# Optimization experiments

Measured on AMD Instinct MI355X. Metric: run time of the kernel, lower is better.

Reference implementation:

```python
import jax, jax.numpy as jnp
import numpy as np

K_TOP = 16
SPLITS = 16


def setup_inputs() -> dict:
    key = jax.random.key(0)
    kq, kt = jax.random.split(key)
    queries = jax.random.normal(kq, (4096, 128), dtype=jnp.float32)
    table = jax.random.normal(kt, (4096, 128, 128), dtype=jnp.float32)
    return {"queries": queries, "table": table}


def reference(queries, table):
    n_queries, vector_dim = queries.shape
    rows, scores_per_row, _ = table.shape
    table_size = rows * scores_per_row
    queries_per_split = n_queries // SPLITS
    q_split = queries.reshape(SPLITS, queries_per_split, vector_dim)
    row_offsets = jnp.arange(0, table_size, scores_per_row)  # [rows]

    def split_top_k(split_queries):
        # scores: [q, rows, values_per_row]
        split_scores = jnp.einsum('qd,rvd->qrv', split_queries, table)
        top_id_by_row = jnp.argmax(split_scores, axis=-1)        # [q, rows]
        top_score_by_row = jnp.max(split_scores, axis=-1)        # [q, rows]
        # top-k rows by per-row max score (descending)
        top_row_idx = jnp.argsort(top_score_by_row, axis=-1)[:, :-K_TOP - 1:-1]  # [q, k]
        # matmul_slice == gather along axis -1 (one-hot matmul trick on TPU)
        ids_by_topk_row = jnp.take_along_axis(top_id_by_row, top_row_idx, axis=-1)  # [q, k]
        split_topk_values = table[top_row_idx, ids_by_topk_row]  # [q, k, d]
        top_table_id_by_row = top_id_by_row + row_offsets        # [q, rows]
        split_topk_ids = jnp.take_along_axis(top_table_id_by_row, top_row_idx, axis=-1)
        split_topk_scores = jnp.take_along_axis(top_score_by_row, top_row_idx, axis=-1)
        return split_topk_values, split_topk_scores, split_topk_ids

    topk_values, topk_scores, topk_ids = jax.lax.map(split_top_k, q_split)
    topk_values = topk_values.reshape(n_queries, K_TOP, -1)
    topk_scores = topk_scores.reshape(n_queries, K_TOP)
    topk_ids = topk_ids.reshape(n_queries, K_TOP)
    return topk_values, topk_scores, topk_ids
```

## Files before the change

### kernel.cpp

```cpp
#include <hip/hip_runtime.h>
#include <stdint.h>


typedef __attribute__((ext_vector_type(8))) short short8;
typedef __attribute__((ext_vector_type(4))) float floatx4;
typedef __attribute__((ext_vector_type(16))) float floatx16;
typedef unsigned long long u64;
typedef unsigned int u32;

#define NQ 4096
#define NR 4096
#define NV 128
#define ND 128
#define KTOP 16
#define RC 16
#define NCHUNK (NR / RC)
#define CPC 8
#define CSEL 24
#define BCAP 1024

__device__ __forceinline__ unsigned short f2bf(float f) {
  u32 u = __float_as_uint(f);
  u32 r = u + 0x7FFFu + ((u >> 16) & 1u);
  return (unsigned short)(r >> 16);
}
__device__ __forceinline__ u32 key_of(float s) {
  u32 b = __float_as_uint(s);
  return (b & 0x80000000u) ? ~b : (b | 0x80000000u);
}
__device__ __forceinline__ float unkey(u32 k) {
  u32 b = (k & 0x80000000u) ? (k & 0x7FFFFFFFu) : ~k;
  return __uint_as_float(b);
}
__device__ __forceinline__ void glds16(const void* g, void* l) {
  __builtin_amdgcn_global_load_lds(
      (const __attribute__((address_space(1))) unsigned int*)g,
      (__attribute__((address_space(3))) unsigned int*)l, 16, 0, 0);
}
__device__ __forceinline__ float max16(floatx16 a) {
  float m0 = fmaxf(fmaxf(a[0], a[1]), fmaxf(a[2], a[3]));
  float m1 = fmaxf(fmaxf(a[4], a[5]), fmaxf(a[6], a[7]));
  float m2 = fmaxf(fmaxf(a[8], a[9]), fmaxf(a[10], a[11]));
  float m3 = fmaxf(fmaxf(a[12], a[13]), fmaxf(a[14], a[15]));
  return fmaxf(fmaxf(m0, m1), fmaxf(m2, m3));
}
__device__ __forceinline__ void insert8(u64* a, u64 x) {
  if (x > a[CPC - 1]) {
#pragma unroll
    for (int p = 0; p < CPC; p++) {
      u64 mx = a[p] > x ? a[p] : x;
      u64 mn = a[p] > x ? x : a[p];
      a[p] = mx; x = mn;
    }
  }
}

__global__ void k0_convert(const float* __restrict__ t, unsigned short* __restrict__ o) {
  size_t i = ((size_t)blockIdx.x * 256 + threadIdx.x) * 4;
  float4 v = *reinterpret_cast<const float4*>(t + i);
  ushort4 r;
  r.x = f2bf(v.x); r.y = f2bf(v.y); r.z = f2bf(v.z); r.w = f2bf(v.w);
  *reinterpret_cast<ushort4*>(o + i) = r;
}

__launch_bounds__(256, 2)
__global__ void k1_coarse(const float* __restrict__ Q, const unsigned short* __restrict__ T16,
                          u64* __restrict__ cand) {
  __shared__ short Blds[2][128 * 128];

  const int tid = threadIdx.x;
  const int wave = tid >> 6;
  const int lane = tid & 63;
  const int l31 = lane & 31;
  const int l15 = lane & 15;
  const int half = lane >> 5;
  const int qblock = blockIdx.x;
  const int chunk = blockIdx.y;

  short8 bf0[8], bf1[8];
  {
    const float* qp0 = Q + (size_t)(qblock * 256 + wave * 64 + l31) * 128;
    const float* qp1 = qp0 + 32 * 128;
#pragma unroll
    for (int kb = 0; kb < 8; kb++) {
      float4 x = *reinterpret_cast<const float4*>(qp0 + kb * 16 + half * 8);
      float4 y = *reinterpret_cast<const float4*>(qp0 + kb * 16 + half * 8 + 4);
      short8 b;
      b[0] = (short)f2bf(x.x); b[1] = (short)f2bf(x.y);
      b[2] = (short)f2bf(x.z); b[3] = (short)f2bf(x.w);
      b[4] = (short)f2bf(y.x); b[5] = (short)f2bf(y.y);
      b[6] = (short)f2bf(y.z); b[7] = (short)f2bf(y.w);
      bf0[kb] = b;
      x = *reinterpret_cast<const float4*>(qp1 + kb * 16 + half * 8);
      y = *reinterpret_cast<const float4*>(qp1 + kb * 16 + half * 8 + 4);
      b[0] = (short)f2bf(x.x); b[1] = (short)f2bf(x.y);
      b[2] = (short)f2bf(x.z); b[3] = (short)f2bf(x.w);
      b[4] = (short)f2bf(y.x); b[5] = (short)f2bf(y.y);
      b[6] = (short)f2bf(y.z); b[7] = (short)f2bf(y.w);
      bf1[kb] = b;
    }
  }

  int goff[8];
#pragma unroll
  for (int i = 0; i < 8; i++) {
    int v = wave * 32 + i * 4 + (lane >> 4);
    int kb = l15 ^ (v & 15);
    goff[i] = v * 256 + kb * 16;
  }
  const char* chunkbase = (const char*)(T16 + (size_t)(chunk * RC) * (NV * ND));

#pragma unroll
  for (int i = 0; i < 8; i++)
    glds16(chunkbase + goff[i], &Blds[0][(wave * 8 + i) * 512 + lane * 8]);
  __syncthreads();

  u64 a0[CPC], a1[CPC];
#pragma unroll
  for (int i = 0; i < CPC; i++) { a0[i] = 0; a1[i] = 0; }

  const short* abase = &Blds[0][l31 * 128];
  for (int rl = 0; rl < RC; rl++) {
    const int cur = rl & 1;
    if (rl < RC - 1) {
      const char* rs = chunkbase + (size_t)(rl + 1) * 32768;
#pragma unroll
      for (int i = 0; i < 8; i++)
        glds16(rs + goff[i], &Blds[1 - cur][(wave * 8 + i) * 512 + lane * 8]);
    }

    float run0 = -3.402823466e+38f, run1 = -3.402823466e+38f;
#pragma unroll
    for (int t = 0; t < 4; t++) {
      floatx16 acc0 = 0, acc1 = 0;
#pragma unroll
      for (int kb = 0; kb < 8; kb++) {
        const short* ap = abase + cur * 16384 + t * 4096 +
                          8 * ((kb * 2 + half) ^ (l31 & 15));
        short8 af = *reinterpret_cast<const short8*>(ap);
        acc0 = __builtin_amdgcn_mfma_f32_32x32x16_bf16(af, bf0[kb], acc0, 0, 0, 0);
        acc1 = __builtin_amdgcn_mfma_f32_32x32x16_bf16(af, bf1[kb], acc1, 0, 0, 0);
      }
      run0 = fmaxf(run0, max16(acc0));
      run1 = fmaxf(run1, max16(acc1));
    }
    run0 = fmaxf(run0, __shfl_xor(run0, 32, 64));
    run1 = fmaxf(run1, __shfl_xor(run1, 32, 64));

    u32 rid = (u32)(chunk * RC + rl);
    insert8(a0, ((u64)key_of(run0) << 32) | rid);
    insert8(a1, ((u64)key_of(run1) << 32) | rid);
    __syncthreads();
  }

  if (lane < 32) {
    const int q0 = qblock * 256 + wave * 64 + l31;
    u64* dst0 = cand + (size_t)q0 * (NCHUNK * CPC) + chunk * CPC;
    u64* dst1 = dst0 + (size_t)32 * (NCHUNK * CPC);
#pragma unroll
    for (int i = 0; i < CPC; i++) { dst0[i] = a0[i]; dst1[i] = a1[i]; }
  }
}

__global__ void k2_select(const u64* __restrict__ cand, u64* __restrict__ refined,
                          u32* __restrict__ cnt, u32* __restrict__ bucket) {
  const int q = blockIdx.x;
  const int lane = threadIdx.x;
  const u64* base = cand + (size_t)q * (NCHUNK * CPC);
  u64 a[12];
#pragma unroll
  for (int i = 0; i < 12; i++) a[i] = 0;
  for (int i = 0; i < 32; i++) {
    u64 x = base[i * 64 + lane];
    if (x > a[11]) {
#pragma unroll
      for (int p = 0; p < 12; p++) {
        u64 mx = a[p] > x ? a[p] : x;
        u64 mn = a[p] > x ? x : a[p];
        a[p] = mx; x = mn;
      }
    }
  }
  if (lane < CSEL) refined[(size_t)q * CSEL + lane] = 0;

  for (int j = 0; j < CSEL; j++) {
    u64 head = a[0];
    u64 W = head;
#pragma unroll
    for (int off = 1; off < 64; off <<= 1) {
      u64 o = __shfl_xor(W, off, 64);
      if (o > W) W = o;
    }
    if (head == W) {
#pragma unroll
      for (int p = 0; p < 11; p++) a[p] = a[p + 1];
      a[11] = 0;
      u32 row = (u32)W & 4095u;
      u32 slot = atomicAdd(cnt + row, 1u);
      if (slot < BCAP) bucket[(size_t)row * BCAP + slot] = ((u32)q << 5) | (u32)j;
    }
  }
}

__device__ __forceinline__ void k3_emit(float acc, u32 ent, int row, int v, int lane,
                                        u64* __restrict__ refined) {
  u64 p = ((u64)key_of(acc) << 32) | (u32)(127 - v);
#pragma unroll
  for (int off = 1; off < 64; off <<= 1) {
    u64 o = __shfl_xor(p, off, 64);
    if (o > p) p = o;
  }
  if (lane == 0) {
    u32 q = ent >> 5, j = ent & 31u;
    u32 vbest = 127u - (u32)(p & 0xFFFFFFFFu);
    u64 packed = ((p >> 32) << 32) | (u32)(row * 128 + vbest);
    atomicMax(reinterpret_cast<unsigned long long*>(&refined[(size_t)q * CSEL + j]), packed);
  }
}

__global__ void k3_refine(const float* __restrict__ Q, const float* __restrict__ table,
                          const u32* __restrict__ cnt, const u32* __restrict__ bucket,
                          u64* __restrict__ refined) {
  __shared__ float rowv[128 * 128];
  const int row = blockIdx.x;
  const int tid = threadIdx.x;
  u32 n = cnt[row];
  if (n > BCAP) n = BCAP;
  if (n == 0) return;
  const float* src = table + (size_t)row * (NV * ND);
#pragma unroll
  for (int i = 0; i < 16; i++) {
    int idx = i * 1024 + tid * 4;
    int v = idx >> 7;
    int d4 = tid & 31;
    *reinterpret_cast<float4*>(&rowv[v * 128 + ((d4 ^ (v & 31)) << 2)]) =
        *reinterpret_cast<const float4*>(src + idx);
  }
  __syncthreads();
  const int g = tid >> 7;
  const int v = tid & 127;
  const int lane = tid & 63;
  const int sw = v & 31;
  const u32* bk = bucket + (size_t)row * BCAP;
  for (u32 e0 = (u32)(g * 4); e0 < n; e0 += 8) {
    u32 ent0 = __builtin_amdgcn_readfirstlane(bk[e0]);
    u32 ent1 = __builtin_amdgcn_readfirstlane(bk[e0 + 1 < n ? e0 + 1 : e0]);
    u32 ent2 = __builtin_amdgcn_readfirstlane(bk[e0 + 2 < n ? e0 + 2 : e0]);
    u32 ent3 = __builtin_amdgcn_readfirstlane(bk[e0 + 3 < n ? e0 + 3 : e0]);
    const float* qp0 = Q + (size_t)(ent0 >> 5) * 128;
    const float* qp1 = Q + (size_t)(ent1 >> 5) * 128;
    const float* qp2 = Q + (size_t)(ent2 >> 5) * 128;
    const float* qp3 = Q + (size_t)(ent3 >> 5) * 128;
    float c0 = 0.f, c1 = 0.f, c2 = 0.f, c3 = 0.f;
#pragma unroll
    for (int d4 = 0; d4 < 32; d4++) {
      float4 rv = *reinterpret_cast<const float4*>(&rowv[v * 128 + ((d4 ^ sw) << 2)]);
      c0 = fmaf(rv.x, qp0[d4 * 4 + 0], c0);
      c0 = fmaf(rv.y, qp0[d4 * 4 + 1], c0);
      c0 = fmaf(rv.z, qp0[d4 * 4 + 2], c0);
      c0 = fmaf(rv.w, qp0[d4 * 4 + 3], c0);
      c1 = fmaf(rv.x, qp1[d4 * 4 + 0], c1);
      c1 = fmaf(rv.y, qp1[d4 * 4 + 1], c1);
      c1 = fmaf(rv.z, qp1[d4 * 4 + 2], c1);
      c1 = fmaf(rv.w, qp1[d4 * 4 + 3], c1);
      c2 = fmaf(rv.x, qp2[d4 * 4 + 0], c2);
      c2 = fmaf(rv.y, qp2[d4 * 4 + 1], c2);
      c2 = fmaf(rv.z, qp2[d4 * 4 + 2], c2);
      c2 = fmaf(rv.w, qp2[d4 * 4 + 3], c2);
      c3 = fmaf(rv.x, qp3[d4 * 4 + 0], c3);
      c3 = fmaf(rv.y, qp3[d4 * 4 + 1], c3);
      c3 = fmaf(rv.z, qp3[d4 * 4 + 2], c3);
      c3 = fmaf(rv.w, qp3[d4 * 4 + 3], c3);
    }
    k3_emit(c0, ent0, row, v, lane, refined);
    if (e0 + 1 < n) k3_emit(c1, ent1, row, v, lane, refined);
    if (e0 + 2 < n) k3_emit(c2, ent2, row, v, lane, refined);
    if (e0 + 3 < n) k3_emit(c3, ent3, row, v, lane, refined);
  }
}

__global__ void k4_finalize(const float* __restrict__ table, const u64* __restrict__ refined,
                            float* __restrict__ out) {
  __shared__ u64 arr[CSEL];
  __shared__ u32 fids[KTOP];
  __shared__ float scs[KTOP];
  const int q = blockIdx.x;
  const int tid = threadIdx.x;
  if (tid < CSEL) arr[tid] = refined[(size_t)q * CSEL + tid];
  __syncthreads();
  if (tid == 0) {
    for (int i = 1; i < CSEL; i++) {
      u64 x = arr[i]; int p = i;
      while (p > 0 && arr[p - 1] < x) { arr[p] = arr[p - 1]; p--; }
      arr[p] = x;
    }
    for (int i = 0; i < KTOP; i++) {
      fids[i] = (u32)arr[i];
      scs[i] = unkey((u32)(arr[i] >> 32));
    }
  }
  __syncthreads();
  const int i = tid >> 4, sub = tid & 15;
  const float* src = table + (size_t)fids[i] * 128 + sub * 8;
  float* dst = out + ((size_t)q * KTOP + i) * 128 + sub * 8;
  *reinterpret_cast<float4*>(dst) = *reinterpret_cast<const float4*>(src);
  *reinterpret_cast<float4*>(dst + 4) = *reinterpret_cast<const float4*>(src + 4);
  if (tid < KTOP) {
    out[8388608 + (size_t)q * KTOP + tid] = scs[tid];
    out[8388608 + 65536 + (size_t)q * KTOP + tid] = (float)fids[tid];
  }
}

extern "C" void kernel_launch(void* const* d_in, const int* in_sizes, int n_in,
                              void* d_out, int out_size, void* d_ws, size_t ws_size,
                              hipStream_t stream) {
  (void)in_sizes; (void)n_in; (void)out_size; (void)ws_size;
  const float* Q = (const float*)d_in[0];
  const float* T = (const float*)d_in[1];
  float* out = (float*)d_out;
  char* ws = (char*)d_ws;
  unsigned short* T16 = (unsigned short*)ws;
  u64* cand    = (u64*)(ws + 134217728);
  u32* cnt     = (u32*)(ws + 134217728 + 67108864);
  u32* bucket  = (u32*)(ws + 134217728 + 67108864 + 16384);
  u64* refined = (u64*)(ws + 134217728 + 67108864 + 16384 + 16777216);

  hipMemsetAsync(cnt, 0, NR * sizeof(u32), stream);
  k0_convert<<<65536, 256, 0, stream>>>(T, T16);
  k1_coarse<<<dim3(16, 256), 256, 0, stream>>>(Q, T16, cand);
  k2_select<<<NQ, 64, 0, stream>>>(cand, refined, cnt, bucket);
  k3_refine<<<NR, 256, 0, stream>>>(Q, T, cnt, bucket, refined);
  k4_finalize<<<NQ, 256, 0, stream>>>(T, refined, out);
}
```

Baseline: 1.316 ms.

## Raise MFMA wave priority in coarse kernel; refine one entry per wave-group with 512 threads

The coarse-scoring kernel now raises wave priority around its MFMA inner loop so that matrix issue is favoured over the other waves. The refine kernel moves from 256 threads, where each 128-thread group handled four bucket entries at once, to 512 threads where each group handles a single entry per iteration. This gives more concurrent waves and less register pressure, but each shared-memory row read is reused across fewer queries. The tile load loop is adjusted to match the larger block.

Result: faster. 1.184 ms (-10.1%).

```diff
diff --git a/kernel.cpp b/kernel.cpp
--- a/kernel.cpp
+++ b/kernel.cpp
@@ -133,6 +133,7 @@
 #pragma unroll
     for (int t = 0; t < 4; t++) {
       floatx16 acc0 = 0, acc1 = 0;
+      __builtin_amdgcn_s_setprio(1);
 #pragma unroll
       for (int kb = 0; kb < 8; kb++) {
         const short* ap = abase + cur * 16384 + t * 4096 +
@@ -141,6 +142,7 @@
         acc0 = __builtin_amdgcn_mfma_f32_32x32x16_bf16(af, bf0[kb], acc0, 0, 0, 0);
         acc1 = __builtin_amdgcn_mfma_f32_32x32x16_bf16(af, bf1[kb], acc1, 0, 0, 0);
       }
+      __builtin_amdgcn_s_setprio(0);
       run0 = fmaxf(run0, max16(acc0));
       run1 = fmaxf(run1, max16(acc1));
     }
@@ -199,22 +201,6 @@
       u32 slot = atomicAdd(cnt + row, 1u);
       if (slot < BCAP) bucket[(size_t)row * BCAP + slot] = ((u32)q << 5) | (u32)j;
     }
-  }
-}
-
-__device__ __forceinline__ void k3_emit(float acc, u32 ent, int row, int v, int lane,
-                                        u64* __restrict__ refined) {
-  u64 p = ((u64)key_of(acc) << 32) | (u32)(127 - v);
-#pragma unroll
-  for (int off = 1; off < 64; off <<= 1) {
-    u64 o = __shfl_xor(p, off, 64);
-    if (o > p) p = o;
-  }
-  if (lane == 0) {
-    u32 q = ent >> 5, j = ent & 31u;
-    u32 vbest = 127u - (u32)(p & 0xFFFFFFFFu);
-    u64 packed = ((p >> 32) << 32) | (u32)(row * 128 + vbest);
-    atomicMax(reinterpret_cast<unsigned long long*>(&refined[(size_t)q * CSEL + j]), packed);
   }
 }
 
@@ -229,53 +215,41 @@
   if (n == 0) return;
   const float* src = table + (size_t)row * (NV * ND);
 #pragma unroll
-  for (int i = 0; i < 16; i++) {
-    int idx = i * 1024 + tid * 4;
+  for (int i = 0; i < 8; i++) {
+    int idx = i * 2048 + tid * 4;
     int v = idx >> 7;
     int d4 = tid & 31;
     *reinterpret_cast<float4*>(&rowv[v * 128 + ((d4 ^ (v & 31)) << 2)]) =
         *reinterpret_cast<const float4*>(src + idx);
   }
   __syncthreads();
-  const int g = tid >> 7;
   const int v = tid & 127;
   const int lane = tid & 63;
   const int sw = v & 31;
-  const u32* bk = bucket + (size_t)row * BCAP;
-  for (u32 e0 = (u32)(g * 4); e0 < n; e0 += 8) {
-    u32 ent0 = __builtin_amdgcn_readfirstlane(bk[e0]);
-    u32 ent1 = __builtin_amdgcn_readfirstlane(bk[e0 + 1 < n ? e0 + 1 : e0]);
-    u32 ent2 = __builtin_amdgcn_readfirstlane(bk[e0 + 2 < n ? e0 + 2 : e0]);
-    u32 ent3 = __builtin_amdgcn_readfirstlane(bk[e0 + 3 < n ? e0 + 3 : e0]);
-    const float* qp0 = Q + (size_t)(ent0 >> 5) * 128;
-    const float* qp1 = Q + (size_t)(ent1 >> 5) * 128;
-    const float* qp2 = Q + (size_t)(ent2 >> 5) * 128;
-    const float* qp3 = Q + (size_t)(ent3 >> 5) * 128;
-    float c0 = 0.f, c1 = 0.f, c2 = 0.f, c3 = 0.f;
+  for (u32 ei = (u32)(tid >> 7); ei < n; ei += 4) {
+    u32 ent = __builtin_amdgcn_readfirstlane(bucket[(size_t)row * BCAP + ei]);
+    u32 q = ent >> 5, j = ent & 31u;
+    const float* qp = Q + (size_t)q * 128;
+    float acc = 0.f;
 #pragma unroll
     for (int d4 = 0; d4 < 32; d4++) {
       float4 rv = *reinterpret_cast<const float4*>(&rowv[v * 128 + ((d4 ^ sw) << 2)]);
-      c0 = fmaf(rv.x, qp0[d4 * 4 + 0], c0);
-      c0 = fmaf(rv.y, qp0[d4 * 4 + 1], c0);
-      c0 = fmaf(rv.z, qp0[d4 * 4 + 2], c0);
-      c0 = fmaf(rv.w, qp0[d4 * 4 + 3], c0);
-      c1 = fmaf(rv.x, qp1[d4 * 4 + 0], c1);
-      c1 = fmaf(rv.y, qp1[d4 * 4 + 1], c1);
-      c1 = fmaf(rv.z, qp1[d4 * 4 + 2], c1);
-      c1 = fmaf(rv.w, qp1[d4 * 4 + 3], c1);
-      c2 = fmaf(rv.x, qp2[d4 * 4 + 0], c2);
-      c2 = fmaf(rv.y, qp2[d4 * 4 + 1], c2);
-      c2 = fmaf(rv.z, qp2[d4 * 4 + 2], c2);
-      c2 = fmaf(rv.w, qp2[d4 * 4 + 3], c2);
-      c3 = fmaf(rv.x, qp3[d4 * 4 + 0], c3);
-      c3 = fmaf(rv.y, qp3[d4 * 4 + 1], c3);
-      c3 = fmaf(rv.z, qp3[d4 * 4 + 2], c3);
-      c3 = fmaf(rv.w, qp3[d4 * 4 + 3], c3);
-    }
-    k3_emit(c0, ent0, row, v, lane, refined);
-    if (e0 + 1 < n) k3_emit(c1, ent1, row, v, lane, refined);
-    if (e0 + 2 < n) k3_emit(c2, ent2, row, v, lane, refined);
-    if (e0 + 3 < n) k3_emit(c3, ent3, row, v, lane, refined);
+      acc = fmaf(rv.x, qp[d4 * 4 + 0], acc);
+      acc = fmaf(rv.y, qp[d4 * 4 + 1], acc);
+      acc = fmaf(rv.z, qp[d4 * 4 + 2], acc);
+      acc = fmaf(rv.w, qp[d4 * 4 + 3], acc);
+    }
+    u64 p = ((u64)key_of(acc) << 32) | (u32)(127 - v);
+#pragma unroll
+    for (int off = 1; off < 64; off <<= 1) {
+      u64 o = __shfl_xor(p, off, 64);
+      if (o > p) p = o;
+    }
+    if (lane == 0) {
+      u32 vbest = 127u - (u32)(p & 0xFFFFFFFFu);
+      u64 packed = ((p >> 32) << 32) | (u32)(row * 128 + vbest);
+      atomicMax(reinterpret_cast<unsigned long long*>(&refined[(size_t)q * CSEL + j]), packed);
+    }
   }
 }
 
@@ -329,6 +303,6 @@
   k0_convert<<<65536, 256, 0, stream>>>(T, T16);
   k1_coarse<<<dim3(16, 256), 256, 0, stream>>>(Q, T16, cand);
   k2_select<<<NQ, 64, 0, stream>>>(cand, refined, cnt, bucket);
-  k3_refine<<<NR, 256, 0, stream>>>(Q, T, cnt, bucket, refined);
+  k3_refine<<<NR, 512, 0, stream>>>(Q, T, cnt, bucket, refined);
   k4_finalize<<<NQ, 256, 0, stream>>>(T, refined, out);
 }
```
